# Kernel tuning notes

Hardware: AMD Instinct MI355X
Metric: run time of the kernel (lower is better)

## Reference

```python
import jax, jax.numpy as jnp
import numpy as np
from jax import lax

KSIZE = 7
SIGMA = 5.0
ALPHA = 0.05


def _gaussian_kernel(ksize: int, sigma: float) -> jnp.ndarray:
    # 2D Gaussian, normalized to sum 1, replicated depthwise for 3 channels: (3,1,k,k)
    ax = jnp.arange(ksize, dtype=jnp.float32) - (ksize - 1) / 2.0
    g1 = jnp.exp(-(ax ** 2) / (2.0 * sigma ** 2))
    g2 = jnp.outer(g1, g1)
    g2 = g2 / jnp.sum(g2)
    return jnp.broadcast_to(g2[None, None], (3, 1, ksize, ksize)).astype(jnp.float32)


def _sobel_kernel() -> jnp.ndarray:
    # (2,1,3,3): channel 0 -> Ix, channel 1 -> Iy
    sx = jnp.array([[-1.0, 0.0, 1.0], [-2.0, 0.0, 2.0], [-1.0, 0.0, 1.0]], dtype=jnp.float32)
    sy = sx.T
    return jnp.stack([sx[None], sy[None]], axis=0)  # (2,1,3,3)


def setup_inputs() -> dict:
    key = jax.random.key(0)
    x = jax.random.normal(key, (1, 1, 4096, 4096), dtype=jnp.float32)
    return {"x": x, "sobel_k": _sobel_kernel(), "gauss_k": _gaussian_kernel(KSIZE, SIGMA)}


def _conv(x, k, pad, groups):
    return lax.conv_general_dilated(
        x, k, window_strides=(1, 1), padding=[(pad, pad), (pad, pad)],
        dimension_numbers=("NCHW", "OIHW", "NCHW"), feature_group_count=groups)


def reference(x, sobel_k, gauss_k):
    # ImageGradientsLayer: Sobel conv -> (1,2,H,W)
    g = _conv(x, sobel_k, 1, 1)
    Ix, Iy = g[:, 0:1], g[:, 1:2]
    # ChannelProductLayer -> (1,3,H,W)
    prod = jnp.concatenate([Ix * Ix, Iy * Iy, Ix * Iy], axis=1)
    # SecondMomentMatrixLayer: depthwise Gaussian blur, groups=3
    S = _conv(prod, gauss_k, KSIZE // 2, 3)
    Sxx, Syy, Sxy = S[0, 0], S[0, 1], S[0, 2]
    # CornerResponseLayer: R = det - alpha*trace^2
    tr = Sxx + Syy
    R = (Sxx * Syy - Sxy * Sxy - ALPHA * tr * tr)[None, None]  # (1,1,H,W)
    # NMSLayer: median threshold, 7x7 maxpool (stride 1, pad 3), keep maxima
    med = jnp.median(R)
    Rt = jnp.where(R >= med, R, jnp.float32(0.0))
    mp = lax.reduce_window(Rt, -jnp.inf, lax.max, (1, 1, 7, 7), (1, 1, 1, 1),
                           [(0, 0), (0, 0), (3, 3), (3, 3)])
    out = jnp.where(Rt != mp, jnp.float32(0.0), mp)
    return out
```

## Files before the change

### kernel.cpp

```cpp
#include <hip/hip_runtime.h>
#include <math.h>

#define N_IMG 4096
#define NBC   1024
#define H_OUT 32
#define HR    38

struct W7 { float w[7]; };

__device__ __forceinline__ unsigned f2k(float f) {
    unsigned u = __float_as_uint(f);
    return (u & 0x80000000u) ? ~u : (u | 0x80000000u);
}
__device__ __forceinline__ float k2f(unsigned k) {
    unsigned u = (k & 0x80000000u) ? (k & 0x7fffffffu) : ~k;
    return __uint_as_float(u);
}

__global__ __launch_bounds__(256) void harris_kernel(const float* __restrict__ x,
                                                     float* __restrict__ R,
                                                     unsigned* __restrict__ ghist,
                                                     W7 wp)
{
    __shared__ unsigned histo[4096];
    const int tid = threadIdx.x;
    for (int i = tid; i < 4096; i += 256) histo[i] = 0;
    __syncthreads();

    const int row0 = blockIdx.y * H_OUT;
    const int jc   = blockIdx.x * NBC + tid * 4;
    const float* w = wp.w;

    float xm[12], xc[12], xp[12];
    float hxx[7][4], hyy[7][4], hxy[7][4];

    auto loadrow = [&](int ri, float* d) {
        if ((unsigned)ri < N_IMG) {
            const float* p = x + (size_t)ri * N_IMG;
            float4 v0 = make_float4(0.f,0.f,0.f,0.f), v2 = make_float4(0.f,0.f,0.f,0.f);
            if (jc >= 4) v0 = *(const float4*)(p + jc - 4);
            float4 v1 = *(const float4*)(p + jc);
            if (jc + 4 < N_IMG) v2 = *(const float4*)(p + jc + 4);
            d[0]=v0.x; d[1]=v0.y; d[2]=v0.z; d[3]=v0.w;
            d[4]=v1.x; d[5]=v1.y; d[6]=v1.z; d[7]=v1.w;
            d[8]=v2.x; d[9]=v2.y; d[10]=v2.z; d[11]=v2.w;
        } else {
            #pragma unroll
            for (int t = 0; t < 12; t++) d[t] = 0.f;
        }
    };

    loadrow(row0 - 4, xm);
    loadrow(row0 - 3, xc);

    int curb = -1; unsigned cnt = 0;

    for (int it = 0; it < 6; ++it) {
        #pragma unroll
        for (int k = 0; k < 7; ++k) {
            const int r = it * 7 + k;
            if (r < HR) {
                const int ri = row0 + r - 3;
                loadrow(ri + 1, xp);

                float sxx[4] = {0,0,0,0}, syy[4] = {0,0,0,0}, sxy[4] = {0,0,0,0};
                if ((unsigned)ri < N_IMG) {
                    float dc[12], rd[12];
                    #pragma unroll
                    for (int t = 0; t < 12; t++) {
                        dc[t] = xm[t] + 2.f * xc[t] + xp[t];
                        rd[t] = xp[t] - xm[t];
                    }
                    #pragma unroll
                    for (int t = 0; t < 10; t++) {
                        float ix = dc[t+2] - dc[t];
                        float iy = rd[t] + 2.f * rd[t+1] + rd[t+2];
                        if ((unsigned)(jc - 3 + t) >= N_IMG) { ix = 0.f; iy = 0.f; }
                        float xx = ix*ix, yy = iy*iy, xy = ix*iy;
                        #pragma unroll
                        for (int o = 0; o < 4; o++) {
                            int v = t - o;
                            if (v >= 0 && v < 7) {
                                sxx[o] = fmaf(w[v], xx, sxx[o]);
                                syy[o] = fmaf(w[v], yy, syy[o]);
                                sxy[o] = fmaf(w[v], xy, sxy[o]);
                            }
                        }
                    }
                }
                #pragma unroll
                for (int o = 0; o < 4; o++) {
                    hxx[k][o] = sxx[o]; hyy[k][o] = syy[o]; hxy[k][o] = sxy[o];
                }

                if (r >= 6) {
                    float4 h;
                    float* hp = &h.x;
                    #pragma unroll
                    for (int o = 0; o < 4; o++) {
                        float ax = 0.f, ay = 0.f, az = 0.f;
                        #pragma unroll
                        for (int u = 0; u < 7; u++) {
                            const int s = (k + 1 + u) % 7;
                            ax = fmaf(w[u], hxx[s][o], ax);
                            ay = fmaf(w[u], hyy[s][o], ay);
                            az = fmaf(w[u], hxy[s][o], az);
                        }
                        float tr = ax + ay;
                        hp[o] = ax*ay - az*az - 0.05f*tr*tr;
                    }
                    const int orow = row0 + r - 6;
                    *(float4*)(R + (size_t)orow * N_IMG + jc) = h;
                    #pragma unroll
                    for (int o = 0; o < 4; o++) {
                        int b = (int)(f2k(hp[o]) >> 20);
                        if (b == curb) cnt++;
                        else { if (curb >= 0) atomicAdd(&histo[curb], cnt); curb = b; cnt = 1; }
                    }
                }
                #pragma unroll
                for (int t = 0; t < 12; t++) { xm[t] = xc[t]; xc[t] = xp[t]; }
            }
        }
    }
    if (curb >= 0) atomicAdd(&histo[curb], cnt);
    __syncthreads();
    for (int i = tid; i < 4096; i += 256) {
        unsigned c = histo[i];
        if (c) atomicAdd(&ghist[i], c);
    }
}

__global__ __launch_bounds__(256) void hist_kernel(const float* __restrict__ R,
                                                   unsigned* __restrict__ ghist,
                                                   const unsigned* __restrict__ state,
                                                   unsigned mask, int shift, int bins)
{
    __shared__ unsigned h[2][4096];
    const int tid = threadIdx.x;
    for (int i = tid; i < 8192; i += 256) ((unsigned*)h)[i] = 0;
    __syncthreads();
    const unsigned p1 = state[0], p2 = state[1];
    const bool dual = (p1 != p2);
    const int n4 = (N_IMG * N_IMG) / 4;
    int curb1 = -1; unsigned cnt1 = 0;
    int curb2 = -1; unsigned cnt2 = 0;
    const float4* R4 = (const float4*)R;
    for (int i = blockIdx.x * 256 + tid; i < n4; i += gridDim.x * 256) {
        float4 v = R4[i];
        float vv[4] = {v.x, v.y, v.z, v.w};
        #pragma unroll
        for (int t = 0; t < 4; t++) {
            unsigned k = f2k(vv[t]);
            if ((k & mask) == p1) {
                int b = (int)((k >> shift) & (unsigned)(bins - 1));
                if (b == curb1) cnt1++;
                else { if (cnt1) atomicAdd(&h[0][curb1], cnt1); curb1 = b; cnt1 = 1; }
            }
            if (dual && (k & mask) == p2) {
                int b = (int)((k >> shift) & (unsigned)(bins - 1));
                if (b == curb2) cnt2++;
                else { if (cnt2) atomicAdd(&h[1][curb2], cnt2); curb2 = b; cnt2 = 1; }
            }
        }
    }
    if (cnt1) atomicAdd(&h[0][curb1], cnt1);
    if (cnt2) atomicAdd(&h[1][curb2], cnt2);
    __syncthreads();
    for (int i = tid; i < bins; i += 256) {
        unsigned c0 = h[0][i]; if (c0) atomicAdd(&ghist[i], c0);
        if (dual) { unsigned c1 = h[1][i]; if (c1) atomicAdd(&ghist[4096 + i], c1); }
    }
}

__global__ __launch_bounds__(256) void select_kernel(unsigned* __restrict__ ghist,
                                                     unsigned* __restrict__ state,
                                                     int shift, int bins, int last)
{
    __shared__ unsigned scan[256];
    __shared__ unsigned res_b[2], res_r[2];
    const int tid = threadIdx.x;
    const int per = bins >> 8;
    unsigned p1 = state[0], p2 = state[1];
    unsigned r1 = state[2], r2 = state[3];
    const bool dual = (p1 != p2);

    for (int q = 0; q < 2; q++) {
        const unsigned* h = (q == 1 && dual) ? (ghist + 4096) : ghist;
        const unsigned rank = (q == 0) ? r1 : r2;
        const int base = tid * per;
        unsigned s = 0;
        for (int i = 0; i < per; i++) s += h[base + i];
        scan[tid] = s;
        __syncthreads();
        unsigned v = s;
        #pragma unroll
        for (int off = 1; off < 256; off <<= 1) {
            unsigned t = (tid >= off) ? scan[tid - off] : 0u;
            __syncthreads();
            v += t;
            scan[tid] = v;
            __syncthreads();
        }
        const unsigned excl = v - s;
        if (rank >= excl && rank < v) {
            unsigned rr = rank - excl;
            unsigned b = (unsigned)base;
            for (int i = 0; i < per; i++) {
                unsigned c = h[base + i];
                if (rr < c) { b = (unsigned)(base + i); break; }
                rr -= c;
            }
            res_b[q] = b; res_r[q] = rr;
        }
        __syncthreads();
    }
    if (tid == 0) {
        p1 |= res_b[0] << shift;  r1 = res_r[0];
        p2 |= res_b[1] << shift;  r2 = res_r[1];
        state[0] = p1; state[1] = p2; state[2] = r1; state[3] = r2;
        if (last) {
            float a = k2f(p1), b = k2f(p2);
            ((float*)state)[4] = 0.5f * (a + b);
        }
    }
    __syncthreads();
    for (int i = tid; i < 8192; i += 256) ghist[i] = 0;
}

__global__ __launch_bounds__(256) void init_kernel(unsigned* __restrict__ ghist,
                                                   unsigned* __restrict__ state)
{
    const int tid = threadIdx.x;
    for (int i = tid; i < 8192; i += 256) ghist[i] = 0;
    if (tid == 0) {
        state[0] = 0u; state[1] = 0u;
        state[2] = 8388607u;
        state[3] = 8388608u;
        state[4] = 0u;
    }
}

__global__ __launch_bounds__(256) void nms_kernel(const float* __restrict__ R,
                                                  const unsigned* __restrict__ state,
                                                  float* __restrict__ out)
{
    const int tid  = threadIdx.x;
    const int row0 = blockIdx.y * H_OUT;
    const int jc   = blockIdx.x * NBC + tid * 4;
    const float med = ((const float*)state)[4];

    float hm[7][4], ct[7][4];

    for (int it = 0; it < 6; ++it) {
        #pragma unroll
        for (int k = 0; k < 7; ++k) {
            const int r = it * 7 + k;
            if (r < HR) {
                const int ri = row0 + r - 3;
                float a[12];
                if ((unsigned)ri < N_IMG) {
                    const float* p = R + (size_t)ri * N_IMG;
                    float4 v1 = *(const float4*)(p + jc);
                    a[4] = (v1.x >= med) ? v1.x : 0.f;
                    a[5] = (v1.y >= med) ? v1.y : 0.f;
                    a[6] = (v1.z >= med) ? v1.z : 0.f;
                    a[7] = (v1.w >= med) ? v1.w : 0.f;
                    if (jc >= 4) {
                        float4 v0 = *(const float4*)(p + jc - 4);
                        a[0] = (v0.x >= med) ? v0.x : 0.f;
                        a[1] = (v0.y >= med) ? v0.y : 0.f;
                        a[2] = (v0.z >= med) ? v0.z : 0.f;
                        a[3] = (v0.w >= med) ? v0.w : 0.f;
                    } else { a[0]=a[1]=a[2]=a[3] = -INFINITY; }
                    if (jc + 4 < N_IMG) {
                        float4 v2 = *(const float4*)(p + jc + 4);
                        a[8]  = (v2.x >= med) ? v2.x : 0.f;
                        a[9]  = (v2.y >= med) ? v2.y : 0.f;
                        a[10] = (v2.z >= med) ? v2.z : 0.f;
                        a[11] = (v2.w >= med) ? v2.w : 0.f;
                    } else { a[8]=a[9]=a[10]=a[11] = -INFINITY; }
                } else {
                    #pragma unroll
                    for (int t = 0; t < 12; t++) a[t] = -INFINITY;
                }
                #pragma unroll
                for (int o = 0; o < 4; o++) {
                    float m = a[o+1];
                    #pragma unroll
                    for (int t = 2; t <= 7; t++) m = fmaxf(m, a[o+t]);
                    hm[k][o] = m;
                    ct[k][o] = a[4+o];
                }
                if (r >= 6) {
                    float4 ov;
                    float* op = &ov.x;
                    #pragma unroll
                    for (int o = 0; o < 4; o++) {
                        float m = hm[(k+1) % 7][o];
                        #pragma unroll
                        for (int u = 1; u < 7; u++) m = fmaxf(m, hm[(k+1+u) % 7][o]);
                        float c = ct[(k+4) % 7][o];
                        op[o] = (c != m) ? 0.f : m;
                    }
                    const int orow = row0 + r - 6;
                    *(float4*)(out + (size_t)orow * N_IMG + jc) = ov;
                }
            }
        }
    }
}

extern "C" void kernel_launch(void* const* d_in, const int* in_sizes, int n_in,
                              void* d_out, int out_size, void* d_ws, size_t ws_size,
                              hipStream_t stream)
{
    const float* x = (const float*)d_in[0];
    float* R = (float*)d_ws;
    unsigned* ghist = (unsigned*)((char*)d_ws + (size_t)N_IMG * N_IMG * 4);
    unsigned* state = ghist + 8192;
    float* out = (float*)d_out;

    W7 wp;
    {
        double g[7], s = 0.0;
        for (int i = 0; i < 7; i++) { double ax = (double)i - 3.0; g[i] = exp(-(ax*ax)/50.0); s += g[i]; }
        for (int i = 0; i < 7; i++) wp.w[i] = (float)(g[i] / s);
    }

    dim3 sgrid(N_IMG / NBC, N_IMG / H_OUT);

    init_kernel<<<1, 256, 0, stream>>>(ghist, state);
    harris_kernel<<<sgrid, 256, 0, stream>>>(x, R, ghist, wp);
    select_kernel<<<1, 256, 0, stream>>>(ghist, state, 20, 4096, 0);
    hist_kernel<<<2048, 256, 0, stream>>>(R, ghist, state, 0xFFF00000u, 8, 4096);
    select_kernel<<<1, 256, 0, stream>>>(ghist, state, 8, 4096, 0);
    hist_kernel<<<2048, 256, 0, stream>>>(R, ghist, state, 0xFFFFFF00u, 0, 256);
    select_kernel<<<1, 256, 0, stream>>>(ghist, state, 0, 256, 1);
    nms_kernel<<<sgrid, 256, 0, stream>>>(R, state, out);
}
```

Baseline: 297.7 us.

## Fold select passes into last-block epilogues and prefetch rows ahead

Removes the three single-block select kernel launches by having the last block to finish each harris/hist kernel, detected with an atomic counter, run the radix-select step itself. It also adds two-row-ahead register prefetching in the harris and NMS sliding-window loops so global loads overlap with compute. The cost is more registers (an extra 12-float row buffer) and a serialized tail in the last block. Histogram reads in the epilogue use atomicOr to get coherent values.

```diff
diff --git a/kernel.cpp b/kernel.cpp
--- a/kernel.cpp
+++ b/kernel.cpp
@@ -5,6 +5,8 @@
 #define NBC   1024
 #define H_OUT 32
 #define HR    38
+#define NBLK_STRIP ((N_IMG/NBC)*(N_IMG/H_OUT))
+#define NBLK_HIST  2048
 
 struct W7 { float w[7]; };
 
@@ -17,12 +19,74 @@
     return __uint_as_float(u);
 }
 
+__device__ __forceinline__ void dual_select(unsigned* ghist, unsigned* state,
+                                            int shift, int per, int last,
+                                            unsigned* sscan, unsigned* sres)
+{
+    const int tid = threadIdx.x;
+    unsigned p1 = state[0], p2 = state[1], r1 = state[2], r2 = state[3];
+    const bool dual = (p1 != p2);
+    for (int q = 0; q < 2; q++) {
+        unsigned* h = (q == 1 && dual) ? (ghist + 4096) : ghist;
+        const unsigned rank = q ? r2 : r1;
+        const int base = tid * per;
+        unsigned vals[16];
+        unsigned s = 0;
+        #pragma unroll
+        for (int i = 0; i < 16; i++) {
+            vals[i] = (i < per) ? atomicOr(&h[base + i], 0u) : 0u;
+            s += vals[i];
+        }
+        sscan[tid] = s;
+        __syncthreads();
+        unsigned v = s;
+        #pragma unroll
+        for (int off = 1; off < 256; off <<= 1) {
+            unsigned t = (tid >= off) ? sscan[tid - off] : 0u;
+            __syncthreads();
+            v += t;
+            sscan[tid] = v;
+            __syncthreads();
+        }
+        const unsigned excl = v - s;
+        if (rank >= excl && rank < v) {
+            unsigned rr = rank - excl;
+            unsigned b = (unsigned)base;
+            #pragma unroll
+            for (int i = 0; i < 16; i++) {
+                if (i < per) {
+                    unsigned c = vals[i];
+                    if (rr < c) { b = (unsigned)(base + i); break; }
+                    rr -= c;
+                }
+            }
+            sres[q * 2] = b; sres[q * 2 + 1] = rr;
+        }
+        __syncthreads();
+    }
+    if (tid == 0) {
+        p1 |= sres[0] << shift;  r1 = sres[1];
+        p2 |= sres[2] << shift;  r2 = sres[3];
+        state[0] = p1; state[1] = p2; state[2] = r1; state[3] = r2;
+        if (last) {
+            float a = k2f(p1), b = k2f(p2);
+            ((float*)state)[4] = 0.5f * (a + b);
+        }
+    }
+    __syncthreads();
+    for (int i = tid; i < 8192; i += 256) ghist[i] = 0;
+}
+
 __global__ __launch_bounds__(256) void harris_kernel(const float* __restrict__ x,
                                                      float* __restrict__ R,
                                                      unsigned* __restrict__ ghist,
+                                                     unsigned* __restrict__ state,
                                                      W7 wp)
 {
     __shared__ unsigned histo[4096];
+    __shared__ unsigned sscan[256];
+    __shared__ unsigned sres[4];
+    __shared__ unsigned lastflag;
     const int tid = threadIdx.x;
     for (int i = tid; i < 4096; i += 256) histo[i] = 0;
     __syncthreads();
@@ -31,7 +95,7 @@
     const int jc   = blockIdx.x * NBC + tid * 4;
     const float* w = wp.w;
 
-    float xm[12], xc[12], xp[12];
+    float xm[12], xc[12], xp[12], xn[12];
     float hxx[7][4], hyy[7][4], hxy[7][4];
 
     auto loadrow = [&](int ri, float* d) {
@@ -52,6 +116,8 @@
 
     loadrow(row0 - 4, xm);
     loadrow(row0 - 3, xc);
+    loadrow(row0 - 2, xp);
+    loadrow(row0 - 1, xn);
 
     int curb = -1; unsigned cnt = 0;
 
@@ -61,7 +127,6 @@
             const int r = it * 7 + k;
             if (r < HR) {
                 const int ri = row0 + r - 3;
-                loadrow(ri + 1, xp);
 
                 float sxx[4] = {0,0,0,0}, syy[4] = {0,0,0,0}, sxy[4] = {0,0,0,0};
                 if ((unsigned)ri < N_IMG) {
@@ -119,7 +184,8 @@
                     }
                 }
                 #pragma unroll
-                for (int t = 0; t < 12; t++) { xm[t] = xc[t]; xc[t] = xp[t]; }
+                for (int t = 0; t < 12; t++) { xm[t] = xc[t]; xc[t] = xp[t]; xp[t] = xn[t]; }
+                loadrow(ri + 3, xn);
             }
         }
     }
@@ -129,15 +195,29 @@
         unsigned c = histo[i];
         if (c) atomicAdd(&ghist[i], c);
     }
+    __syncthreads();
+
+    if (tid == 0) {
+        __threadfence();
+        unsigned t = atomicAdd(&state[5], 1u);
+        lastflag = (t == NBLK_STRIP - 1) ? 1u : 0u;
+    }
+    __syncthreads();
+    if (lastflag) dual_select(ghist, state, 20, 16, 0, sscan, sres);
 }
 
 __global__ __launch_bounds__(256) void hist_kernel(const float* __restrict__ R,
                                                    unsigned* __restrict__ ghist,
-                                                   const unsigned* __restrict__ state,
-                                                   unsigned mask, int shift, int bins)
+                                                   unsigned* __restrict__ state,
+                                                   unsigned mask, int shift, int per,
+                                                   int last, int cslot)
 {
     __shared__ unsigned h[2][4096];
+    __shared__ unsigned sscan[256];
+    __shared__ unsigned sres[4];
+    __shared__ unsigned lastflag;
     const int tid = threadIdx.x;
+    const int bins = per << 8;
     for (int i = tid; i < 8192; i += 256) ((unsigned*)h)[i] = 0;
     __syncthreads();
     const unsigned p1 = state[0], p2 = state[1];
@@ -171,61 +251,15 @@
         unsigned c0 = h[0][i]; if (c0) atomicAdd(&ghist[i], c0);
         if (dual) { unsigned c1 = h[1][i]; if (c1) atomicAdd(&ghist[4096 + i], c1); }
     }
-}
-
-__global__ __launch_bounds__(256) void select_kernel(unsigned* __restrict__ ghist,
-                                                     unsigned* __restrict__ state,
-                                                     int shift, int bins, int last)
-{
-    __shared__ unsigned scan[256];
-    __shared__ unsigned res_b[2], res_r[2];
-    const int tid = threadIdx.x;
-    const int per = bins >> 8;
-    unsigned p1 = state[0], p2 = state[1];
-    unsigned r1 = state[2], r2 = state[3];
-    const bool dual = (p1 != p2);
-
-    for (int q = 0; q < 2; q++) {
-        const unsigned* h = (q == 1 && dual) ? (ghist + 4096) : ghist;
-        const unsigned rank = (q == 0) ? r1 : r2;
-        const int base = tid * per;
-        unsigned s = 0;
-        for (int i = 0; i < per; i++) s += h[base + i];
-        scan[tid] = s;
-        __syncthreads();
-        unsigned v = s;
-        #pragma unroll
-        for (int off = 1; off < 256; off <<= 1) {
-            unsigned t = (tid >= off) ? scan[tid - off] : 0u;
-            __syncthreads();
-            v += t;
-            scan[tid] = v;
-            __syncthreads();
-        }
-        const unsigned excl = v - s;
-        if (rank >= excl && rank < v) {
-            unsigned rr = rank - excl;
-            unsigned b = (unsigned)base;
-            for (int i = 0; i < per; i++) {
-                unsigned c = h[base + i];
-                if (rr < c) { b = (unsigned)(base + i); break; }
-                rr -= c;
-            }
-            res_b[q] = b; res_r[q] = rr;
-        }
-        __syncthreads();
-    }
+    __syncthreads();
+
     if (tid == 0) {
-        p1 |= res_b[0] << shift;  r1 = res_r[0];
-        p2 |= res_b[1] << shift;  r2 = res_r[1];
-        state[0] = p1; state[1] = p2; state[2] = r1; state[3] = r2;
-        if (last) {
-            float a = k2f(p1), b = k2f(p2);
-            ((float*)state)[4] = 0.5f * (a + b);
-        }
-    }
-    __syncthreads();
-    for (int i = tid; i < 8192; i += 256) ghist[i] = 0;
+        __threadfence();
+        unsigned t = atomicAdd(&state[cslot], 1u);
+        lastflag = (t == NBLK_HIST - 1) ? 1u : 0u;
+    }
+    __syncthreads();
+    if (lastflag) dual_select(ghist, state, shift, per, last, sscan, sres);
 }
 
 __global__ __launch_bounds__(256) void init_kernel(unsigned* __restrict__ ghist,
@@ -238,6 +272,7 @@
         state[2] = 8388607u;
         state[3] = 8388608u;
         state[4] = 0u;
+        state[5] = 0u; state[6] = 0u; state[7] = 0u;
     }
 }
 
@@ -249,8 +284,31 @@
     const int row0 = blockIdx.y * H_OUT;
     const int jc   = blockIdx.x * NBC + tid * 4;
     const float med = ((const float*)state)[4];
-
+    const bool leftok  = (jc >= 4);
+    const bool rightok = (jc + 4 < N_IMG);
+
+    float cur[12], nx1[12], nx2[12];
     float hm[7][4], ct[7][4];
+
+    auto loadraw = [&](int ri, float* d) {
+        if ((unsigned)ri < N_IMG) {
+            const float* p = R + (size_t)ri * N_IMG;
+            float4 v0 = make_float4(0.f,0.f,0.f,0.f), v2 = make_float4(0.f,0.f,0.f,0.f);
+            if (leftok)  v0 = *(const float4*)(p + jc - 4);
+            float4 v1 = *(const float4*)(p + jc);
+            if (rightok) v2 = *(const float4*)(p + jc + 4);
+            d[0]=v0.x; d[1]=v0.y; d[2]=v0.z; d[3]=v0.w;
+            d[4]=v1.x; d[5]=v1.y; d[6]=v1.z; d[7]=v1.w;
+            d[8]=v2.x; d[9]=v2.y; d[10]=v2.z; d[11]=v2.w;
+        } else {
+            #pragma unroll
+            for (int t = 0; t < 12; t++) d[t] = 0.f;
+        }
+    };
+
+    loadraw(row0 - 3, cur);
+    loadraw(row0 - 2, nx1);
+    loadraw(row0 - 1, nx2);
 
     for (int it = 0; it < 6; ++it) {
         #pragma unroll
@@ -258,31 +316,14 @@
             const int r = it * 7 + k;
             if (r < HR) {
                 const int ri = row0 + r - 3;
+                const bool rowok = ((unsigned)ri < N_IMG);
                 float a[12];
-                if ((unsigned)ri < N_IMG) {
-                    const float* p = R + (size_t)ri * N_IMG;
-                    float4 v1 = *(const float4*)(p + jc);
-                    a[4] = (v1.x >= med) ? v1.x : 0.f;
-                    a[5] = (v1.y >= med) ? v1.y : 0.f;
-                    a[6] = (v1.z >= med) ? v1.z : 0.f;
-                    a[7] = (v1.w >= med) ? v1.w : 0.f;
-                    if (jc >= 4) {
-                        float4 v0 = *(const float4*)(p + jc - 4);
-                        a[0] = (v0.x >= med) ? v0.x : 0.f;
-                        a[1] = (v0.y >= med) ? v0.y : 0.f;
-                        a[2] = (v0.z >= med) ? v0.z : 0.f;
-                        a[3] = (v0.w >= med) ? v0.w : 0.f;
-                    } else { a[0]=a[1]=a[2]=a[3] = -INFINITY; }
-                    if (jc + 4 < N_IMG) {
-                        float4 v2 = *(const float4*)(p + jc + 4);
-                        a[8]  = (v2.x >= med) ? v2.x : 0.f;
-                        a[9]  = (v2.y >= med) ? v2.y : 0.f;
-                        a[10] = (v2.z >= med) ? v2.z : 0.f;
-                        a[11] = (v2.w >= med) ? v2.w : 0.f;
-                    } else { a[8]=a[9]=a[10]=a[11] = -INFINITY; }
-                } else {
-                    #pragma unroll
-                    for (int t = 0; t < 12; t++) a[t] = -INFINITY;
+                #pragma unroll
+                for (int t = 0; t < 12; t++) {
+                    float v = cur[t];
+                    float thr = (v >= med) ? v : 0.f;
+                    bool colok = (t < 4) ? leftok : ((t < 8) ? true : rightok);
+                    a[t] = (rowok && colok) ? thr : -INFINITY;
                 }
                 #pragma unroll
                 for (int o = 0; o < 4; o++) {
@@ -306,6 +347,9 @@
                     const int orow = row0 + r - 6;
                     *(float4*)(out + (size_t)orow * N_IMG + jc) = ov;
                 }
+                #pragma unroll
+                for (int t = 0; t < 12; t++) { cur[t] = nx1[t]; nx1[t] = nx2[t]; }
+                loadraw(ri + 3, nx2);
             }
         }
     }
@@ -331,11 +375,8 @@
     dim3 sgrid(N_IMG / NBC, N_IMG / H_OUT);
 
     init_kernel<<<1, 256, 0, stream>>>(ghist, state);
-    harris_kernel<<<sgrid, 256, 0, stream>>>(x, R, ghist, wp);
-    select_kernel<<<1, 256, 0, stream>>>(ghist, state, 20, 4096, 0);
-    hist_kernel<<<2048, 256, 0, stream>>>(R, ghist, state, 0xFFF00000u, 8, 4096);
-    select_kernel<<<1, 256, 0, stream>>>(ghist, state, 8, 4096, 0);
-    hist_kernel<<<2048, 256, 0, stream>>>(R, ghist, state, 0xFFFFFF00u, 0, 256);
-    select_kernel<<<1, 256, 0, stream>>>(ghist, state, 0, 256, 1);
+    harris_kernel<<<sgrid, 256, 0, stream>>>(x, R, ghist, state, wp);
+    hist_kernel<<<NBLK_HIST, 256, 0, stream>>>(R, ghist, state, 0xFFF00000u, 8, 16, 0, 6);
+    hist_kernel<<<NBLK_HIST, 256, 0, stream>>>(R, ghist, state, 0xFFFFFF00u, 0, 1, 1, 7);
     nms_kernel<<<sgrid, 256, 0, stream>>>(R, state, out);
 }
```

Result: slower. 352.3 us (+18.4%).

## Compact radix-select candidates during second pass and fuse final selection

Applied to the files above, without the earlier changes.

During the second histogram pass, elements matching the current median prefix are staged in shared memory and appended to a global candidate buffer. The final radix pass then histograms only those candidates instead of rescanning all of R, and the last finishing block performs the final selection, removing a separate select launch. A full-image fallback handles buffer overflow. This adds per-iteration block synchronisation and shared atomics to the second pass, and larger shared memory use.

```diff
diff --git a/kernel.cpp b/kernel.cpp
--- a/kernel.cpp
+++ b/kernel.cpp
@@ -5,6 +5,8 @@
 #define NBC   1024
 #define H_OUT 32
 #define HR    38
+#define NBLK_HIST 2048
+#define STAGE_CAP 4096
 
 struct W7 { float w[7]; };
 
@@ -131,48 +133,6 @@
     }
 }
 
-__global__ __launch_bounds__(256) void hist_kernel(const float* __restrict__ R,
-                                                   unsigned* __restrict__ ghist,
-                                                   const unsigned* __restrict__ state,
-                                                   unsigned mask, int shift, int bins)
-{
-    __shared__ unsigned h[2][4096];
-    const int tid = threadIdx.x;
-    for (int i = tid; i < 8192; i += 256) ((unsigned*)h)[i] = 0;
-    __syncthreads();
-    const unsigned p1 = state[0], p2 = state[1];
-    const bool dual = (p1 != p2);
-    const int n4 = (N_IMG * N_IMG) / 4;
-    int curb1 = -1; unsigned cnt1 = 0;
-    int curb2 = -1; unsigned cnt2 = 0;
-    const float4* R4 = (const float4*)R;
-    for (int i = blockIdx.x * 256 + tid; i < n4; i += gridDim.x * 256) {
-        float4 v = R4[i];
-        float vv[4] = {v.x, v.y, v.z, v.w};
-        #pragma unroll
-        for (int t = 0; t < 4; t++) {
-            unsigned k = f2k(vv[t]);
-            if ((k & mask) == p1) {
-                int b = (int)((k >> shift) & (unsigned)(bins - 1));
-                if (b == curb1) cnt1++;
-                else { if (cnt1) atomicAdd(&h[0][curb1], cnt1); curb1 = b; cnt1 = 1; }
-            }
-            if (dual && (k & mask) == p2) {
-                int b = (int)((k >> shift) & (unsigned)(bins - 1));
-                if (b == curb2) cnt2++;
-                else { if (cnt2) atomicAdd(&h[1][curb2], cnt2); curb2 = b; cnt2 = 1; }
-            }
-        }
-    }
-    if (cnt1) atomicAdd(&h[0][curb1], cnt1);
-    if (cnt2) atomicAdd(&h[1][curb2], cnt2);
-    __syncthreads();
-    for (int i = tid; i < bins; i += 256) {
-        unsigned c0 = h[0][i]; if (c0) atomicAdd(&ghist[i], c0);
-        if (dual) { unsigned c1 = h[1][i]; if (c1) atomicAdd(&ghist[4096 + i], c1); }
-    }
-}
-
 __global__ __launch_bounds__(256) void select_kernel(unsigned* __restrict__ ghist,
                                                      unsigned* __restrict__ state,
                                                      int shift, int bins, int last)
@@ -228,6 +188,171 @@
     for (int i = tid; i < 8192; i += 256) ghist[i] = 0;
 }
 
+__global__ __launch_bounds__(256) void hist1rec_kernel(const float* __restrict__ R,
+                                                       unsigned* __restrict__ ghist,
+                                                       unsigned* __restrict__ state,
+                                                       unsigned* __restrict__ rec,
+                                                       unsigned reccap)
+{
+    __shared__ unsigned h[2][4096];
+    __shared__ unsigned stage[STAGE_CAP];
+    __shared__ unsigned scount, sbase, soflow;
+    const int tid = threadIdx.x;
+    for (int i = tid; i < 8192; i += 256) ((unsigned*)h)[i] = 0;
+    if (tid == 0) { scount = 0; soflow = 0; }
+    __syncthreads();
+
+    const unsigned p1 = state[0], p2 = state[1];
+    const bool dual = (p1 != p2);
+    int curb1 = -1; unsigned cnt1 = 0;
+    int curb2 = -1; unsigned cnt2 = 0;
+    const float4* R4 = (const float4*)R;
+    const int n4 = (N_IMG * N_IMG) / 4;
+    const int stride = NBLK_HIST * 256;
+
+    for (int ii = 0; ii < n4 / stride; ii++) {
+        int i = blockIdx.x * 256 + tid + ii * stride;
+        float4 v = R4[i];
+        float vv[4] = {v.x, v.y, v.z, v.w};
+        #pragma unroll
+        for (int t = 0; t < 4; t++) {
+            unsigned k = f2k(vv[t]);
+            bool m1 = ((k & 0xFFF00000u) == p1);
+            bool m2 = dual && ((k & 0xFFF00000u) == p2);
+            if (m1) {
+                int b = (int)((k >> 8) & 4095u);
+                if (b == curb1) cnt1++;
+                else { if (cnt1) atomicAdd(&h[0][curb1], cnt1); curb1 = b; cnt1 = 1; }
+            }
+            if (m2) {
+                int b = (int)((k >> 8) & 4095u);
+                if (b == curb2) cnt2++;
+                else { if (cnt2) atomicAdd(&h[1][curb2], cnt2); curb2 = b; cnt2 = 1; }
+            }
+            if (m1 || m2) {
+                unsigned s = atomicAdd(&scount, 1u);
+                if (s < STAGE_CAP) stage[s] = k;
+                else soflow = 1u;
+            }
+        }
+        __syncthreads();
+        if (scount > STAGE_CAP - 1024) {
+            if (tid == 0) sbase = atomicAdd(&state[6], scount);
+            __syncthreads();
+            unsigned n = (scount < STAGE_CAP) ? scount : STAGE_CAP;
+            for (unsigned j = tid; j < n; j += 256) {
+                unsigned gi = sbase + j;
+                if (gi < reccap) rec[gi] = stage[j];
+                else soflow = 1u;
+            }
+            __syncthreads();
+            if (tid == 0) scount = 0;
+            __syncthreads();
+        }
+    }
+    __syncthreads();
+    if (scount > 0) {
+        if (tid == 0) sbase = atomicAdd(&state[6], scount);
+        __syncthreads();
+        unsigned n = (scount < STAGE_CAP) ? scount : STAGE_CAP;
+        for (unsigned j = tid; j < n; j += 256) {
+            unsigned gi = sbase + j;
+            if (gi < reccap) rec[gi] = stage[j];
+            else soflow = 1u;
+        }
+        __syncthreads();
+    }
+    if (cnt1) atomicAdd(&h[0][curb1], cnt1);
+    if (cnt2) atomicAdd(&h[1][curb2], cnt2);
+    if (tid == 0 && soflow) atomicOr(&state[7], 1u);
+    __syncthreads();
+    for (int i = tid; i < 4096; i += 256) {
+        unsigned c0 = h[0][i]; if (c0) atomicAdd(&ghist[i], c0);
+        if (dual) { unsigned c1 = h[1][i]; if (c1) atomicAdd(&ghist[4096 + i], c1); }
+    }
+}
+
+__global__ __launch_bounds__(256) void selfinal_kernel(const float* __restrict__ R,
+                                                       unsigned* __restrict__ ghist,
+                                                       unsigned* __restrict__ state,
+                                                       const unsigned* __restrict__ rec)
+{
+    __shared__ unsigned h0[256], h1[256];
+    __shared__ unsigned sscan[256];
+    __shared__ unsigned sres[4];
+    __shared__ unsigned lastflag;
+    const int tid = threadIdx.x;
+    h0[tid] = 0; h1[tid] = 0;
+    __syncthreads();
+
+    const unsigned p1 = state[0], p2 = state[1];
+    const bool dual = (p1 != p2);
+    const unsigned oflow = state[7];
+
+    if (!oflow) {
+        const unsigned n = state[6];
+        for (unsigned i = blockIdx.x * 256 + tid; i < n; i += NBLK_HIST * 256) {
+            unsigned k = rec[i];
+            unsigned pre = k & 0xFFFFFF00u;
+            if (pre == p1) atomicAdd(&h0[k & 255u], 1u);
+            else if (dual && pre == p2) atomicAdd(&h1[k & 255u], 1u);
+        }
+    } else {
+        const float4* R4 = (const float4*)R;
+        const int n4 = (N_IMG * N_IMG) / 4;
+        for (int i = blockIdx.x * 256 + tid; i < n4; i += NBLK_HIST * 256) {
+            float4 v = R4[i];
+            float vv[4] = {v.x, v.y, v.z, v.w};
+            #pragma unroll
+            for (int t = 0; t < 4; t++) {
+                unsigned k = f2k(vv[t]);
+                unsigned pre = k & 0xFFFFFF00u;
+                if (pre == p1) atomicAdd(&h0[k & 255u], 1u);
+                else if (dual && pre == p2) atomicAdd(&h1[k & 255u], 1u);
+            }
+        }
+    }
+    __syncthreads();
+    { unsigned c = h0[tid]; if (c) atomicAdd(&ghist[tid], c); }
+    if (dual) { unsigned c = h1[tid]; if (c) atomicAdd(&ghist[4096 + tid], c); }
+    __syncthreads();
+
+    if (tid == 0) {
+        __threadfence();
+        unsigned t = atomicAdd(&state[5], 1u);
+        lastflag = (t == NBLK_HIST - 1) ? 1u : 0u;
+    }
+    __syncthreads();
+    if (!lastflag) return;
+
+    unsigned q1 = state[0], q2 = state[1], r1 = state[2], r2 = state[3];
+    for (int q = 0; q < 2; q++) {
+        unsigned* hh = (q == 1 && dual) ? (ghist + 4096) : ghist;
+        const unsigned rank = q ? r2 : r1;
+        unsigned s = atomicOr(&hh[tid], 0u);
+        sscan[tid] = s;
+        __syncthreads();
+        unsigned v = s;
+        #pragma unroll
+        for (int off = 1; off < 256; off <<= 1) {
+            unsigned t = (tid >= off) ? sscan[tid - off] : 0u;
+            __syncthreads();
+            v += t;
+            sscan[tid] = v;
+            __syncthreads();
+        }
+        const unsigned excl = v - s;
+        if (rank >= excl && rank < v) { sres[q * 2] = (unsigned)tid; sres[q * 2 + 1] = rank - excl; }
+        __syncthreads();
+    }
+    if (tid == 0) {
+        q1 |= sres[0];  q2 |= sres[2];
+        state[0] = q1; state[1] = q2; state[2] = sres[1]; state[3] = sres[3];
+        float a = k2f(q1), b = k2f(q2);
+        ((float*)state)[4] = 0.5f * (a + b);
+    }
+}
+
 __global__ __launch_bounds__(256) void init_kernel(unsigned* __restrict__ ghist,
                                                    unsigned* __restrict__ state)
 {
@@ -238,6 +363,9 @@
         state[2] = 8388607u;
         state[3] = 8388608u;
         state[4] = 0u;
+        state[5] = 0u;
+        state[6] = 0u;
+        state[7] = 0u;
     }
 }
 
@@ -316,9 +444,17 @@
                               hipStream_t stream)
 {
     const float* x = (const float*)d_in[0];
+    const size_t R_BYTES = (size_t)N_IMG * N_IMG * 4;
     float* R = (float*)d_ws;
-    unsigned* ghist = (unsigned*)((char*)d_ws + (size_t)N_IMG * N_IMG * 4);
+    unsigned* ghist = (unsigned*)((char*)d_ws + R_BYTES);
     unsigned* state = ghist + 8192;
+    const size_t recOff = R_BYTES + 40960;
+    unsigned* rec = (unsigned*)((char*)d_ws + recOff);
+    unsigned reccap = 0;
+    if (ws_size > recOff + 4) {
+        size_t c = (ws_size - recOff) / 4;
+        reccap = (c > 8u * 1024 * 1024) ? 8u * 1024 * 1024 : (unsigned)c;
+    }
     float* out = (float*)d_out;
 
     W7 wp;
@@ -333,9 +469,8 @@
     init_kernel<<<1, 256, 0, stream>>>(ghist, state);
     harris_kernel<<<sgrid, 256, 0, stream>>>(x, R, ghist, wp);
     select_kernel<<<1, 256, 0, stream>>>(ghist, state, 20, 4096, 0);
-    hist_kernel<<<2048, 256, 0, stream>>>(R, ghist, state, 0xFFF00000u, 8, 4096);
+    hist1rec_kernel<<<NBLK_HIST, 256, 0, stream>>>(R, ghist, state, rec, reccap);
     select_kernel<<<1, 256, 0, stream>>>(ghist, state, 8, 4096, 0);
-    hist_kernel<<<2048, 256, 0, stream>>>(R, ghist, state, 0xFFFFFF00u, 0, 256);
-    select_kernel<<<1, 256, 0, stream>>>(ghist, state, 0, 256, 1);
+    selfinal_kernel<<<NBLK_HIST, 256, 0, stream>>>(R, ghist, state, rec);
     nms_kernel<<<sgrid, 256, 0, stream>>>(R, state, out);
 }
```

New measurement: 334.5 us. 12.4% more time.
